# Kernel tuning notes

Hardware: AMD Instinct MI355X
Metric: run time of the kernel (lower is better)

## Reference

```python
import jax, jax.numpy as jnp
import numpy as np

N = 10000        # nodes
E = 320000       # edges (before self-loops)
G = 100          # graphs in batch
HEADS = 2
OUT = 125        # per-head out channels
NEG_SLOPE = 0.2  # PyG GATConv default leaky_relu slope


def setup_inputs() -> dict:
    key = jax.random.key(0)
    k = lambda i: jax.random.fold_in(key, i)
    rn = lambda i, shape, s=0.1: jax.random.normal(k(i), shape, jnp.float32) * s
    inp = {
        "x": jax.random.normal(k(0), (N, 336), jnp.float32),
        "edge_index": jax.random.randint(k(1), (2, E), 0, N, jnp.int32),
        "batch": jnp.sort(jax.random.randint(k(2), (N,), 0, G, jnp.int32)),
    }
    conv_in = [336, 250, 250, 250]
    for i, din in enumerate(conv_in, start=1):
        base = 10 * i
        inp[f"W{i}"] = rn(base, (din, HEADS * OUT))
        inp[f"asrc{i}"] = rn(base + 1, (HEADS, OUT))
        inp[f"adst{i}"] = rn(base + 2, (HEADS, OUT))
        inp[f"b{i}"] = jnp.zeros((HEADS * OUT,), jnp.float32)
    lin_dims = [(250, 200), (200, 100), (100, 100), (100, 29)]
    for i, (din, dout) in enumerate(lin_dims, start=1):
        inp[f"lw{i}"] = rn(100 + i, (din, dout))
        inp[f"lb{i}"] = jnp.zeros((dout,), jnp.float32)
    return inp


def gat_conv(x, src, dst, W, asrc, adst, b):
    # PyG GATConv (v1), concat heads, self-loops already in (src, dst).
    n = x.shape[0]
    h = (x @ W).reshape(n, HEADS, OUT)                    # [N,H,C]
    e_src = jnp.einsum('nhc,hc->nh', h, asrc)             # a_src . h_j
    e_dst = jnp.einsum('nhc,hc->nh', h, adst)             # a_dst . h_i
    e = jax.nn.leaky_relu(e_src[src] + e_dst[dst], NEG_SLOPE)  # [Etot,H]
    m = jax.ops.segment_max(e, dst, num_segments=n)       # segment softmax over incoming edges
    e = jnp.exp(e - m[dst])
    denom = jax.ops.segment_sum(e, dst, num_segments=n)
    alpha = e / (denom[dst] + 1e-16)                      # [Etot,H]
    out = jax.ops.segment_sum(alpha[:, :, None] * h[src], dst, num_segments=n)
    return out.reshape(n, HEADS * OUT) + b


def reference(x, edge_index, batch,
              W1, asrc1, adst1, b1, W2, asrc2, adst2, b2,
              W3, asrc3, adst3, b3, W4, asrc4, adst4, b4,
              lw1, lb1, lw2, lb2, lw3, lb3, lw4, lb4):
    n = x.shape[0]
    loop = jnp.arange(n, dtype=edge_index.dtype)
    src = jnp.concatenate([edge_index[0], loop])          # add_self_loops=True
    dst = jnp.concatenate([edge_index[1], loop])

    h = jax.nn.relu(gat_conv(x, src, dst, W1, asrc1, adst1, b1))
    h = jax.nn.relu(gat_conv(h, src, dst, W2, asrc2, adst2, b2))
    h = jax.nn.relu(gat_conv(h, src, dst, W3, asrc3, adst3, b3))
    h = jax.nn.relu(gat_conv(h, src, dst, W4, asrc4, adst4, b4))

    # global_mean_pool over graph ids
    sums = jax.ops.segment_sum(h, batch, num_segments=G)
    cnts = jax.ops.segment_sum(jnp.ones((n, 1), h.dtype), batch, num_segments=G)
    g = sums / jnp.maximum(cnts, 1.0)                     # [G,250]

    g = jax.nn.relu(g @ lw1 + lb1)
    g = jax.nn.relu(g @ lw2 + lb2)
    g = jax.nn.relu(g @ lw3 + lb3)
    return g @ lw4 + lb4                                  # [G,29]
```

## Files before the change

### kernel.cpp

```cpp
#include <hip/hip_runtime.h>
#include <hip/hip_bf16.h>

#define NNODES 10000
#define NEDGES 320000
#define ETOT   (NEDGES + NNODES)
#define NGRAPH 100
#define CH     250
#define HOUT   125
#define MPAD   10048
#define NTILE  157
#define KP0    352
#define KP1    256
#define HPAD   256
#define ECAP   128
#define DCAPW  128

typedef __attribute__((ext_vector_type(8))) short bf16x8;
typedef __attribute__((ext_vector_type(4))) float f32x4;

static __device__ __forceinline__ float bfbits2f(unsigned int u){
  union{ unsigned int i; float f; } v; v.i = u << 16; return v.f;
}
static __device__ __forceinline__ unsigned short f2bfbits(float f){
  __hip_bfloat16 b = __float2bfloat16(f);
  union{ __hip_bfloat16 b; unsigned short s; } v; v.b = b; return v.s;
}

struct Args {
  const float* x; const int* eidx; const int* batch;
  const float *W0,*W1,*W2,*W3;
  __hip_bfloat16 *hb16, *Abf0, *Abf, *Wt0, *Wt1, *Wt2, *Wt3;
  int *cursor, *bucket, *gstart;
};

__global__ void k_pre(Args a){
  int gtid = blockIdx.x * blockDim.x + threadIdx.x;
  int gstr = gridDim.x * blockDim.x;
  for (int e = gtid; e < ETOT; e += gstr){
    int dst, src;
    if (e < NEDGES){ src = a.eidx[e]; dst = a.eidx[NEDGES + e]; }
    else           { src = e - NEDGES; dst = src; }
    int pos = atomicAdd(&a.cursor[dst], 1);
    if (pos < ECAP) a.bucket[(size_t)dst * ECAP + pos] = src;
  }
  for (int n = gtid; n < NNODES; n += gstr){
    int b1 = a.batch[n];
    int b0 = (n == 0) ? -1 : a.batch[n-1];
    for (int b = b0 + 1; b <= b1; ++b) a.gstart[b] = n;
    if (n == NNODES - 1){
      for (int b = b1 + 1; b <= NGRAPH; ++b) a.gstart[b] = NNODES;
    }
  }
  for (int i = gtid; i < NNODES*336; i += gstr){
    int r = i / 336, k = i % 336;
    a.Abf0[(size_t)r * KP0 + k] = __float2bfloat16(a.x[i]);
  }
  const int T0 = 16 * KP0 * 16;
  const int T1 = 16 * KP1 * 16;
  int tot = T0 + 3*T1;
  for (int i = gtid; i < tot; i += gstr){
    const float* W; __hip_bfloat16* Wt; int K, Kp, li;
    if (i < T0)             { W = a.W0; Wt = a.Wt0; K = 336; Kp = KP0; li = i; }
    else if (i < T0 +   T1) { W = a.W1; Wt = a.Wt1; K = CH;  Kp = KP1; li = i - T0; }
    else if (i < T0 + 2*T1) { W = a.W2; Wt = a.Wt2; K = CH;  Kp = KP1; li = i - T0 - T1; }
    else                    { W = a.W3; Wt = a.Wt3; K = CH;  Kp = KP1; li = i - T0 - 2*T1; }
    int KC = Kp >> 5;
    int nt = li / (Kp * 16);
    int rem = li % (Kp * 16);
    int k = rem / 16;
    int n = rem % 16;
    int col = nt * 16 + n;
    float v = (k < K && col < CH) ? W[(size_t)k * CH + col] : 0.f;
    Wt[(((size_t)nt * KC + (k >> 5)) * 16 + n) * 32 + (k & 31)] = __float2bfloat16(v);
  }
}

__global__ __launch_bounds__(256) void k_gemm(
    const __hip_bfloat16* __restrict__ A, const __hip_bfloat16* __restrict__ Wt,
    __hip_bfloat16* __restrict__ Cb, const float* __restrict__ asrc,
    const float* __restrict__ adst, float* __restrict__ esrc, float* __restrict__ edst,
    int Kp){
  int wv = threadIdx.x >> 6, lane = threadIdx.x & 63;
  int n16 = lane & 15, q = lane >> 4;
  int KC = Kp >> 5;
  int rowbase = blockIdx.x * 64 + wv * 16;
  int bn = blockIdx.y * 64;
  int nt0 = bn >> 4;
  const __hip_bfloat16* ap = A  + (size_t)(rowbase + n16) * Kp + q * 8;
  const __hip_bfloat16* bp = Wt + ((size_t)nt0 * KC * 16 + n16) * 32 + q * 8;
  f32x4 ac0 = {0.f,0.f,0.f,0.f}, ac1 = ac0, ac2 = ac0, ac3 = ac0;
  for (int kc = 0; kc < KC; ++kc){
    bf16x8 a  = *(const bf16x8*)(ap + (size_t)kc * 32);
    bf16x8 b0 = *(const bf16x8*)(bp + ((size_t)0 * KC + kc) * 512);
    bf16x8 b1 = *(const bf16x8*)(bp + ((size_t)1 * KC + kc) * 512);
    bf16x8 b2 = *(const bf16x8*)(bp + ((size_t)2 * KC + kc) * 512);
    bf16x8 b3 = *(const bf16x8*)(bp + ((size_t)3 * KC + kc) * 512);
    ac0 = __builtin_amdgcn_mfma_f32_16x16x32_bf16(a, b0, ac0, 0, 0, 0);
    ac1 = __builtin_amdgcn_mfma_f32_16x16x32_bf16(a, b1, ac1, 0, 0, 0);
    ac2 = __builtin_amdgcn_mfma_f32_16x16x32_bf16(a, b2, ac2, 0, 0, 0);
    ac3 = __builtin_amdgcn_mfma_f32_16x16x32_bf16(a, b3, ac3, 0, 0, 0);
  }
  float es0[4] = {}, es1[4] = {}, ed0a[4] = {}, ed1a[4] = {};
  #define SCORE_T(AC, T) { \
    int col = bn + (T)*16 + n16; \
    bool ok = col < CH; \
    float av = ok ? asrc[col] : 0.f; \
    float dv = ok ? adst[col] : 0.f; \
    bool hh = col >= HOUT; \
    float av0 = hh ? 0.f : av, av1 = hh ? av : 0.f; \
    float dv0 = hh ? 0.f : dv, dv1 = hh ? dv : 0.f; \
    _Pragma("unroll") \
    for (int r = 0; r < 4; ++r){ \
      es0[r] += AC[r]*av0; es1[r] += AC[r]*av1; \
      ed0a[r] += AC[r]*dv0; ed1a[r] += AC[r]*dv1; } }
  SCORE_T(ac0, 0) SCORE_T(ac1, 1) SCORE_T(ac2, 2) SCORE_T(ac3, 3)
  #undef SCORE_T
  #pragma unroll
  for (int off = 1; off < 16; off <<= 1){
    #pragma unroll
    for (int r = 0; r < 4; ++r){
      es0[r]  += __shfl_xor(es0[r],  off);
      es1[r]  += __shfl_xor(es1[r],  off);
      ed0a[r] += __shfl_xor(ed0a[r], off);
      ed1a[r] += __shfl_xor(ed1a[r], off);
    }
  }
  if (n16 == 0){
    #pragma unroll
    for (int r = 0; r < 4; ++r){
      int row = rowbase + q*4 + r;
      if (row < NNODES){
        atomicAdd(&esrc[row*2+0], es0[r]);
        atomicAdd(&esrc[row*2+1], es1[r]);
        atomicAdd(&edst[row*2+0], ed0a[r]);
        atomicAdd(&edst[row*2+1], ed1a[r]);
      }
    }
  }
  #pragma unroll
  for (int r = 0; r < 4; ++r){
    int row = rowbase + q * 4 + r;
    if (row >= NNODES) continue;
    int col = bn + n16;
    __hip_bfloat16* cb = Cb + (size_t)row * HPAD + col;
    if (col      < CH) cb[0]  = __float2bfloat16(ac0[r]);
    if (col + 16 < CH) cb[16] = __float2bfloat16(ac1[r]);
    if (col + 32 < CH) cb[32] = __float2bfloat16(ac2[r]);
    if (col + 48 < CH) cb[48] = __float2bfloat16(ac3[r]);
  }
}

__global__ __launch_bounds__(256) void k_attn(const __hip_bfloat16* __restrict__ h,
                        const float* __restrict__ esrc, const float* __restrict__ edst,
                        const int* __restrict__ degv, const int* __restrict__ bucket,
                        const float* __restrict__ bias, __hip_bfloat16* __restrict__ outb,
                        float* __restrict__ esZ, float* __restrict__ edZ){
  int wv = threadIdx.x >> 6, lane = threadIdx.x & 63;
  int node = blockIdx.x * 4 + wv;
  __shared__ int   s_src[4][DCAPW];
  __shared__ float s_x0[4][DCAPW], s_x1[4][DCAPW];
  int deg = degv[node]; if (deg > ECAP) deg = ECAP;
  const int* __restrict__ eb = bucket + (size_t)node * ECAP;
  float ed0 = edst[node*2+0], ed1 = edst[node*2+1];
  float sm0 = 0.f, sm1 = 0.f;
  for (int i = lane; i < deg; i += 64){
    int src = eb[i];
    float e0 = esrc[src*2+0] + ed0; e0 = e0 > 0.f ? e0 : 0.2f*e0;
    float e1 = esrc[src*2+1] + ed1; e1 = e1 > 0.f ? e1 : 0.2f*e1;
    float x0 = __expf(e0), x1 = __expf(e1);
    if (i < DCAPW){ s_src[wv][i] = src; s_x0[wv][i] = x0; s_x1[wv][i] = x1; }
    sm0 += x0; sm1 += x1;
  }
  #pragma unroll
  for (int off = 32; off > 0; off >>= 1){
    sm0 += __shfl_xor(sm0, off);
    sm1 += __shfl_xor(sm1, off);
  }
  float inv0 = 1.f / (sm0 + 1e-16f);
  float inv1 = 1.f / (sm1 + 1e-16f);
  __syncthreads();
  int c0 = 4*lane;
  bool h0_0 = (c0    ) < HOUT, h0_1 = (c0 + 1) < HOUT;
  bool h0_2 = (c0 + 2) < HOUT, h0_3 = (c0 + 3) < HOUT;
  float acc0=0.f, acc1=0.f, acc2=0.f, acc3=0.f;
  #define FETCH(I, S, A0, A1) { \
    if ((I) < DCAPW){ S = s_src[wv][I]; A0 = s_x0[wv][I]*inv0; A1 = s_x1[wv][I]*inv1; } \
    else { S = eb[I]; \
      float e0 = esrc[S*2+0] + ed0; e0 = e0 > 0.f ? e0 : 0.2f*e0; \
      float e1 = esrc[S*2+1] + ed1; e1 = e1 > 0.f ? e1 : 0.2f*e1; \
      A0 = __expf(e0)*inv0; A1 = __expf(e1)*inv1; } }
  #define GATHER(S, A0, A1) { \
    uint2 d = *(const uint2*)(h + (size_t)(S) * HPAD + c0); \
    acc0 += (h0_0 ? A0 : A1) * bfbits2f(d.x & 0xffffu); \
    acc1 += (h0_1 ? A0 : A1) * bfbits2f(d.x >> 16); \
    acc2 += (h0_2 ? A0 : A1) * bfbits2f(d.y & 0xffffu); \
    acc3 += (h0_3 ? A0 : A1) * bfbits2f(d.y >> 16); }
  int i = 0;
  for (; i + 1 < deg; i += 2){
    int sA, sB; float a0A,a1A,a0B,a1B;
    FETCH(i, sA, a0A, a1A)
    FETCH(i+1, sB, a0B, a1B)
    GATHER(sA, a0A, a1A)
    GATHER(sB, a0B, a1B)
  }
  if (i < deg){
    int sA; float a0A, a1A;
    FETCH(i, sA, a0A, a1A)
    GATHER(sA, a0A, a1A)
  }
  #undef GATHER
  #undef FETCH
  if (lane < 62){
    float4 b4 = *(const float4*)&bias[c0];
    float v0 = acc0 + b4.x, v1 = acc1 + b4.y, v2 = acc2 + b4.z, v3 = acc3 + b4.w;
    v0 = v0 > 0.f ? v0 : 0.f; v1 = v1 > 0.f ? v1 : 0.f;
    v2 = v2 > 0.f ? v2 : 0.f; v3 = v3 > 0.f ? v3 : 0.f;
    ushort4 o; o.x = f2bfbits(v0); o.y = f2bfbits(v1); o.z = f2bfbits(v2); o.w = f2bfbits(v3);
    *(ushort4*)(outb + (size_t)node * KP1 + c0) = o;
  } else if (lane == 62){
    float v0 = acc0 + bias[248];
    float v1 = acc1 + bias[249];
    v0 = v0 > 0.f ? v0 : 0.f; v1 = v1 > 0.f ? v1 : 0.f;
    outb[(size_t)node * KP1 + 248] = __float2bfloat16(v0);
    outb[(size_t)node * KP1 + 249] = __float2bfloat16(v1);
  }
  if (lane < 2){
    esZ[node*2 + lane] = 0.f;
    edZ[node*2 + lane] = 0.f;
  }
}

__global__ __launch_bounds__(256) void k_head(const __hip_bfloat16* __restrict__ xb,
                        const int* __restrict__ gstart,
                        const float* __restrict__ lw1, const float* __restrict__ lb1,
                        const float* __restrict__ lw2, const float* __restrict__ lb2,
                        const float* __restrict__ lw3, const float* __restrict__ lb3,
                        const float* __restrict__ lw4, const float* __restrict__ lb4,
                        float* __restrict__ out){
  int g = blockIdx.x;
  int tid = threadIdx.x;
  int s = gstart[g], e = gstart[g+1];
  __shared__ float gvec[256];
  __shared__ float m1[200];
  __shared__ float m2[112];
  __shared__ float m3[112];
  if (tid < CH){
    float a0=0.f,a1=0.f,a2=0.f,a3=0.f;
    int n = s;
    for (; n + 3 < e; n += 4){
      a0 += __bfloat162float(xb[(size_t)n     * KP1 + tid]);
      a1 += __bfloat162float(xb[(size_t)(n+1) * KP1 + tid]);
      a2 += __bfloat162float(xb[(size_t)(n+2) * KP1 + tid]);
      a3 += __bfloat162float(xb[(size_t)(n+3) * KP1 + tid]);
    }
    for (; n < e; ++n) a0 += __bfloat162float(xb[(size_t)n * KP1 + tid]);
    float scale = 1.f / fmaxf((float)(e - s), 1.f);
    gvec[tid] = (a0 + a1 + a2 + a3) * scale;
  }
  __syncthreads();
  if (tid < 200){
    float a0=0.f,a1=0.f,a2=0.f,a3=0.f;
    int k = 0;
    for (; k + 3 < CH; k += 4){
      a0 += gvec[k]   * lw1[(size_t)k     * 200 + tid];
      a1 += gvec[k+1] * lw1[(size_t)(k+1) * 200 + tid];
      a2 += gvec[k+2] * lw1[(size_t)(k+2) * 200 + tid];
      a3 += gvec[k+3] * lw1[(size_t)(k+3) * 200 + tid];
    }
    for (; k < CH; ++k) a0 += gvec[k] * lw1[(size_t)k * 200 + tid];
    float v = a0 + a1 + a2 + a3 + lb1[tid];
    m1[tid] = v > 0.f ? v : 0.f;
  }
  __syncthreads();
  if (tid < 100){
    float a0=0.f,a1=0.f,a2=0.f,a3=0.f;
    for (int k = 0; k + 3 < 200; k += 4){
      a0 += m1[k]   * lw2[(size_t)k     * 100 + tid];
      a1 += m1[k+1] * lw2[(size_t)(k+1) * 100 + tid];
      a2 += m1[k+2] * lw2[(size_t)(k+2) * 100 + tid];
      a3 += m1[k+3] * lw2[(size_t)(k+3) * 100 + tid];
    }
    float v = a0 + a1 + a2 + a3 + lb2[tid];
    m2[tid] = v > 0.f ? v : 0.f;
  }
  __syncthreads();
  if (tid < 100){
    float a0=0.f,a1=0.f,a2=0.f,a3=0.f;
    for (int k = 0; k + 3 < 100; k += 4){
      a0 += m2[k]   * lw3[(size_t)k     * 100 + tid];
      a1 += m2[k+1] * lw3[(size_t)(k+1) * 100 + tid];
      a2 += m2[k+2] * lw3[(size_t)(k+2) * 100 + tid];
      a3 += m2[k+3] * lw3[(size_t)(k+3) * 100 + tid];
    }
    float v = a0 + a1 + a2 + a3 + lb3[tid];
    m3[tid] = v > 0.f ? v : 0.f;
  }
  __syncthreads();
  if (tid < 29){
    float a0=0.f,a1=0.f,a2=0.f,a3=0.f;
    for (int k = 0; k + 3 < 100; k += 4){
      a0 += m3[k]   * lw4[(size_t)k     * 29 + tid];
      a1 += m3[k+1] * lw4[(size_t)(k+1) * 29 + tid];
      a2 += m3[k+2] * lw4[(size_t)(k+2) * 29 + tid];
      a3 += m3[k+3] * lw4[(size_t)(k+3) * 29 + tid];
    }
    out[(size_t)g * 29 + tid] = a0 + a1 + a2 + a3 + lb4[tid];
  }
}

extern "C" void kernel_launch(void* const* d_in, const int* in_sizes, int n_in,
                              void* d_out, int out_size, void* d_ws, size_t ws_size,
                              hipStream_t stream){
  char* ws = (char*)d_ws;
  size_t off = 0;
  auto alloc = [&](size_t bytes)->void*{
    void* p = ws + off;
    off = (off + bytes + 255) & ~(size_t)255;
    return p;
  };
  __hip_bfloat16* hb16 = (__hip_bfloat16*)alloc((size_t)NNODES * HPAD * 2);
  __hip_bfloat16* Abf0 = (__hip_bfloat16*)alloc((size_t)MPAD * KP0 * 2);
  __hip_bfloat16* Abf  = (__hip_bfloat16*)alloc((size_t)MPAD * KP1 * 2);
  __hip_bfloat16* Wt0  = (__hip_bfloat16*)alloc((size_t)16 * KP0 * 16 * 2);
  __hip_bfloat16* Wt1  = (__hip_bfloat16*)alloc((size_t)16 * KP1 * 16 * 2);
  __hip_bfloat16* Wt2  = (__hip_bfloat16*)alloc((size_t)16 * KP1 * 16 * 2);
  __hip_bfloat16* Wt3  = (__hip_bfloat16*)alloc((size_t)16 * KP1 * 16 * 2);
  size_t zbeg = off;
  int*   cursor = (int*)  alloc((size_t)NNODES * 4);
  float* esA  = (float*)alloc((size_t)NNODES * 2 * 4);
  float* edA  = (float*)alloc((size_t)NNODES * 2 * 4);
  size_t zend = off;
  float* esB  = (float*)alloc((size_t)NNODES * 2 * 4);
  float* edB  = (float*)alloc((size_t)NNODES * 2 * 4);
  int*   bucket = (int*)alloc((size_t)NNODES * ECAP * 4);
  int*   gstart = (int*)alloc((size_t)(NGRAPH + 1) * 4);

  hipMemsetAsync(ws + zbeg, 0, zend - zbeg, stream);

  Args a;
  a.x = (const float*)d_in[0];
  a.eidx = (const int*)d_in[1];
  a.batch = (const int*)d_in[2];
  a.W0 = (const float*)d_in[3];  a.W1 = (const float*)d_in[7];
  a.W2 = (const float*)d_in[11]; a.W3 = (const float*)d_in[15];
  a.hb16 = hb16; a.Abf0 = Abf0; a.Abf = Abf;
  a.Wt0 = Wt0; a.Wt1 = Wt1; a.Wt2 = Wt2; a.Wt3 = Wt3;
  a.cursor = cursor; a.bucket = bucket; a.gstart = gstart;

  k_pre<<<(ETOT + 255)/256, 256, 0, stream>>>(a);

  const __hip_bfloat16* Wts[4] = {Wt0, Wt1, Wt2, Wt3};
  for (int L = 0; L < 4; ++L){
    const float* as_ = (const float*)d_in[4 + 4*L];
    const float* ad_ = (const float*)d_in[5 + 4*L];
    const float* bb  = (const float*)d_in[6 + 4*L];
    int Kp = (L == 0) ? KP0 : KP1;
    const __hip_bfloat16* Ain = (L == 0) ? Abf0 : Abf;
    float* es  = (L & 1) ? esB : esA;
    float* ed  = (L & 1) ? edB : edA;
    float* esZ = (L & 1) ? esA : esB;
    float* edZ = (L & 1) ? edA : edB;

    k_gemm<<<dim3(NTILE, 4), 256, 0, stream>>>(Ain, Wts[L], hb16, as_, ad_, es, ed, Kp);
    k_attn<<<NNODES/4, 256, 0, stream>>>(hb16, es, ed, cursor, bucket, bb, Abf, esZ, edZ);
  }

  k_head<<<NGRAPH, 256, 0, stream>>>(Abf, gstart,
      (const float*)d_in[19], (const float*)d_in[20],
      (const float*)d_in[21], (const float*)d_in[22],
      (const float*)d_in[23], (const float*)d_in[24],
      (const float*)d_in[25], (const float*)d_in[26],
      (float*)d_out);
}
```

Measured before the change: 318.6 us.

## Widen attention gather to 16-byte loads with split-wave edge parallelism

Restructures the attention aggregation so each half-wave handles alternating edges with 8 bf16 channels per lane loaded as uint4. Partial sums from the two halves are combined with a cross-half shuffle. Softmax normalization moves to after accumulation, the edge score load becomes a float2, and the shared buffers merge into a float2 array. Separately, the GEMM epilogue writes zeros into padded columns, and the mean-pool head reads two bf16 per thread. The global-memory fallback for degree above DCAPW is dropped, which relies on ECAP equalling DCAPW; it also reads the padded h columns, so it depends on them being zeroed.

```diff
diff --git a/kernel.cpp b/kernel.cpp
--- a/kernel.cpp
+++ b/kernel.cpp
@@ -18,8 +18,11 @@
 typedef __attribute__((ext_vector_type(8))) short bf16x8;
 typedef __attribute__((ext_vector_type(4))) float f32x4;
 
-static __device__ __forceinline__ float bfbits2f(unsigned int u){
+static __device__ __forceinline__ float bflo(unsigned int u){
   union{ unsigned int i; float f; } v; v.i = u << 16; return v.f;
+}
+static __device__ __forceinline__ float bfhi(unsigned int u){
+  union{ unsigned int i; float f; } v; v.i = u & 0xffff0000u; return v.f;
 }
 static __device__ __forceinline__ unsigned short f2bfbits(float f){
   __hip_bfloat16 b = __float2bfloat16(f);
@@ -143,10 +146,10 @@
     if (row >= NNODES) continue;
     int col = bn + n16;
     __hip_bfloat16* cb = Cb + (size_t)row * HPAD + col;
-    if (col      < CH) cb[0]  = __float2bfloat16(ac0[r]);
-    if (col + 16 < CH) cb[16] = __float2bfloat16(ac1[r]);
-    if (col + 32 < CH) cb[32] = __float2bfloat16(ac2[r]);
-    if (col + 48 < CH) cb[48] = __float2bfloat16(ac3[r]);
+    cb[0]  = __float2bfloat16(col      < CH ? ac0[r] : 0.f);
+    cb[16] = __float2bfloat16(col + 16 < CH ? ac1[r] : 0.f);
+    cb[32] = __float2bfloat16(col + 32 < CH ? ac2[r] : 0.f);
+    cb[48] = __float2bfloat16(col + 48 < CH ? ac3[r] : 0.f);
   }
 }
 
@@ -157,18 +160,19 @@
                         float* __restrict__ esZ, float* __restrict__ edZ){
   int wv = threadIdx.x >> 6, lane = threadIdx.x & 63;
   int node = blockIdx.x * 4 + wv;
-  __shared__ int   s_src[4][DCAPW];
-  __shared__ float s_x0[4][DCAPW], s_x1[4][DCAPW];
+  __shared__ int    s_src[4][DCAPW];
+  __shared__ float2 s_x[4][DCAPW];
   int deg = degv[node]; if (deg > ECAP) deg = ECAP;
   const int* __restrict__ eb = bucket + (size_t)node * ECAP;
   float ed0 = edst[node*2+0], ed1 = edst[node*2+1];
   float sm0 = 0.f, sm1 = 0.f;
   for (int i = lane; i < deg; i += 64){
     int src = eb[i];
-    float e0 = esrc[src*2+0] + ed0; e0 = e0 > 0.f ? e0 : 0.2f*e0;
-    float e1 = esrc[src*2+1] + ed1; e1 = e1 > 0.f ? e1 : 0.2f*e1;
+    float2 ev = *(const float2*)(esrc + (size_t)src * 2);
+    float e0 = ev.x + ed0; e0 = e0 > 0.f ? e0 : 0.2f*e0;
+    float e1 = ev.y + ed1; e1 = e1 > 0.f ? e1 : 0.2f*e1;
     float x0 = __expf(e0), x1 = __expf(e1);
-    if (i < DCAPW){ s_src[wv][i] = src; s_x0[wv][i] = x0; s_x1[wv][i] = x1; }
+    s_src[wv][i] = src; s_x[wv][i] = make_float2(x0, x1);
     sm0 += x0; sm1 += x1;
   }
   #pragma unroll
@@ -179,50 +183,63 @@
   float inv0 = 1.f / (sm0 + 1e-16f);
   float inv1 = 1.f / (sm1 + 1e-16f);
   __syncthreads();
-  int c0 = 4*lane;
-  bool h0_0 = (c0    ) < HOUT, h0_1 = (c0 + 1) < HOUT;
-  bool h0_2 = (c0 + 2) < HOUT, h0_3 = (c0 + 3) < HOUT;
-  float acc0=0.f, acc1=0.f, acc2=0.f, acc3=0.f;
-  #define FETCH(I, S, A0, A1) { \
-    if ((I) < DCAPW){ S = s_src[wv][I]; A0 = s_x0[wv][I]*inv0; A1 = s_x1[wv][I]*inv1; } \
-    else { S = eb[I]; \
-      float e0 = esrc[S*2+0] + ed0; e0 = e0 > 0.f ? e0 : 0.2f*e0; \
-      float e1 = esrc[S*2+1] + ed1; e1 = e1 > 0.f ? e1 : 0.2f*e1; \
-      A0 = __expf(e0)*inv0; A1 = __expf(e1)*inv1; } }
-  #define GATHER(S, A0, A1) { \
-    uint2 d = *(const uint2*)(h + (size_t)(S) * HPAD + c0); \
-    acc0 += (h0_0 ? A0 : A1) * bfbits2f(d.x & 0xffffu); \
-    acc1 += (h0_1 ? A0 : A1) * bfbits2f(d.x >> 16); \
-    acc2 += (h0_2 ? A0 : A1) * bfbits2f(d.y & 0xffffu); \
-    acc3 += (h0_3 ? A0 : A1) * bfbits2f(d.y >> 16); }
-  int i = 0;
-  for (; i + 1 < deg; i += 2){
-    int sA, sB; float a0A,a1A,a0B,a1B;
-    FETCH(i, sA, a0A, a1A)
-    FETCH(i+1, sB, a0B, a1B)
-    GATHER(sA, a0A, a1A)
-    GATHER(sB, a0B, a1B)
-  }
-  if (i < deg){
-    int sA; float a0A, a1A;
-    FETCH(i, sA, a0A, a1A)
-    GATHER(sA, a0A, a1A)
-  }
-  #undef GATHER
-  #undef FETCH
-  if (lane < 62){
-    float4 b4 = *(const float4*)&bias[c0];
-    float v0 = acc0 + b4.x, v1 = acc1 + b4.y, v2 = acc2 + b4.z, v3 = acc3 + b4.w;
-    v0 = v0 > 0.f ? v0 : 0.f; v1 = v1 > 0.f ? v1 : 0.f;
-    v2 = v2 > 0.f ? v2 : 0.f; v3 = v3 > 0.f ? v3 : 0.f;
-    ushort4 o; o.x = f2bfbits(v0); o.y = f2bfbits(v1); o.z = f2bfbits(v2); o.w = f2bfbits(v3);
-    *(ushort4*)(outb + (size_t)node * KP1 + c0) = o;
-  } else if (lane == 62){
-    float v0 = acc0 + bias[248];
-    float v1 = acc1 + bias[249];
-    v0 = v0 > 0.f ? v0 : 0.f; v1 = v1 > 0.f ? v1 : 0.f;
-    outb[(size_t)node * KP1 + 248] = __float2bfloat16(v0);
-    outb[(size_t)node * KP1 + 249] = __float2bfloat16(v1);
+  int half = lane >> 5, hl = lane & 31;
+  int c0 = hl * 8;
+  int n0 = HOUT - c0; n0 = n0 < 0 ? 0 : (n0 > 8 ? 8 : n0);
+  const __hip_bfloat16* __restrict__ hrow = h + c0;
+  float acc[8] = {0.f,0.f,0.f,0.f,0.f,0.f,0.f,0.f};
+  #define EDGE(IDX) { \
+    bool vld = (IDX) < deg; \
+    int jj = vld ? (IDX) : 0; \
+    int s = s_src[wv][jj]; \
+    float2 xv = s_x[wv][jj]; \
+    float a0 = vld ? xv.x : 0.f; \
+    float a1 = vld ? xv.y : 0.f; \
+    uint4 d = *(const uint4*)(hrow + (size_t)s * HPAD); \
+    acc[0] += (0 < n0 ? a0 : a1) * bflo(d.x); \
+    acc[1] += (1 < n0 ? a0 : a1) * bfhi(d.x); \
+    acc[2] += (2 < n0 ? a0 : a1) * bflo(d.y); \
+    acc[3] += (3 < n0 ? a0 : a1) * bfhi(d.y); \
+    acc[4] += (4 < n0 ? a0 : a1) * bflo(d.z); \
+    acc[5] += (5 < n0 ? a0 : a1) * bfhi(d.z); \
+    acc[6] += (6 < n0 ? a0 : a1) * bflo(d.w); \
+    acc[7] += (7 < n0 ? a0 : a1) * bfhi(d.w); }
+  for (int it = half; it < deg; it += 4){
+    EDGE(it)
+    EDGE(it + 2)
+  }
+  #undef EDGE
+  #pragma unroll
+  for (int j = 0; j < 8; ++j) acc[j] += __shfl_xor(acc[j], 32);
+  if (half == 0){
+    if (hl < 31){
+      float4 bA = *(const float4*)&bias[c0];
+      float4 bB = *(const float4*)&bias[c0 + 4];
+      float v0 = acc[0]*(0 < n0 ? inv0 : inv1) + bA.x;
+      float v1 = acc[1]*(1 < n0 ? inv0 : inv1) + bA.y;
+      float v2 = acc[2]*(2 < n0 ? inv0 : inv1) + bA.z;
+      float v3 = acc[3]*(3 < n0 ? inv0 : inv1) + bA.w;
+      float v4 = acc[4]*(4 < n0 ? inv0 : inv1) + bB.x;
+      float v5 = acc[5]*(5 < n0 ? inv0 : inv1) + bB.y;
+      float v6 = acc[6]*(6 < n0 ? inv0 : inv1) + bB.z;
+      float v7 = acc[7]*(7 < n0 ? inv0 : inv1) + bB.w;
+      v0 = v0 > 0.f ? v0 : 0.f; v1 = v1 > 0.f ? v1 : 0.f;
+      v2 = v2 > 0.f ? v2 : 0.f; v3 = v3 > 0.f ? v3 : 0.f;
+      v4 = v4 > 0.f ? v4 : 0.f; v5 = v5 > 0.f ? v5 : 0.f;
+      v6 = v6 > 0.f ? v6 : 0.f; v7 = v7 > 0.f ? v7 : 0.f;
+      uint4 o;
+      o.x = (unsigned int)f2bfbits(v0) | ((unsigned int)f2bfbits(v1) << 16);
+      o.y = (unsigned int)f2bfbits(v2) | ((unsigned int)f2bfbits(v3) << 16);
+      o.z = (unsigned int)f2bfbits(v4) | ((unsigned int)f2bfbits(v5) << 16);
+      o.w = (unsigned int)f2bfbits(v6) | ((unsigned int)f2bfbits(v7) << 16);
+      *(uint4*)(outb + (size_t)node * KP1 + c0) = o;
+    } else {
+      float v0 = acc[0]*inv1 + bias[248];
+      float v1 = acc[1]*inv1 + bias[249];
+      v0 = v0 > 0.f ? v0 : 0.f; v1 = v1 > 0.f ? v1 : 0.f;
+      unsigned int o = (unsigned int)f2bfbits(v0) | ((unsigned int)f2bfbits(v1) << 16);
+      *(unsigned int*)(outb + (size_t)node * KP1 + 248) = o;
+    }
   }
   if (lane < 2){
     esZ[node*2 + lane] = 0.f;
@@ -244,18 +261,26 @@
   __shared__ float m1[200];
   __shared__ float m2[112];
   __shared__ float m3[112];
-  if (tid < CH){
-    float a0=0.f,a1=0.f,a2=0.f,a3=0.f;
+  if (tid < 128){
+    int c2 = tid * 2;
+    const __hip_bfloat16* xp = xb + c2;
+    float a0=0.f,a1=0.f,b0=0.f,b1=0.f;
     int n = s;
     for (; n + 3 < e; n += 4){
-      a0 += __bfloat162float(xb[(size_t)n     * KP1 + tid]);
-      a1 += __bfloat162float(xb[(size_t)(n+1) * KP1 + tid]);
-      a2 += __bfloat162float(xb[(size_t)(n+2) * KP1 + tid]);
-      a3 += __bfloat162float(xb[(size_t)(n+3) * KP1 + tid]);
-    }
-    for (; n < e; ++n) a0 += __bfloat162float(xb[(size_t)n * KP1 + tid]);
+      unsigned int u0 = *(const unsigned int*)(xp + (size_t)n     * KP1);
+      unsigned int u1 = *(const unsigned int*)(xp + (size_t)(n+1) * KP1);
+      unsigned int u2 = *(const unsigned int*)(xp + (size_t)(n+2) * KP1);
+      unsigned int u3 = *(const unsigned int*)(xp + (size_t)(n+3) * KP1);
+      a0 += bflo(u0) + bflo(u2); a1 += bfhi(u0) + bfhi(u2);
+      b0 += bflo(u1) + bflo(u3); b1 += bfhi(u1) + bfhi(u3);
+    }
+    for (; n < e; ++n){
+      unsigned int u0 = *(const unsigned int*)(xp + (size_t)n * KP1);
+      a0 += bflo(u0); a1 += bfhi(u0);
+    }
     float scale = 1.f / fmaxf((float)(e - s), 1.f);
-    gvec[tid] = (a0 + a1 + a2 + a3) * scale;
+    gvec[c2]     = (a0 + b0) * scale;
+    gvec[c2 + 1] = (a1 + b1) * scale;
   }
   __syncthreads();
   if (tid < 200){
```

After: 303.7 us. 1.05x faster.
